# Optimization experiments

Measured on AMD Instinct MI355X. Metric: run time of the kernel, lower is better.

## Reference

```python
import jax, jax.numpy as jnp
import numpy as np

E = 100000    # number of edges
T = 1000000   # number of triplets
D = 128       # embed_dim
NB = 20       # n_basis (angle expansion width)
EPS = 1e-6


def setup_inputs() -> dict:
    key = jax.random.key(0)
    ks = jax.random.split(key, 14)
    def lin(k, fan_in, fan_out):
        # torch.nn.Linear default init: U(-1/sqrt(fan_in), 1/sqrt(fan_in))
        bound = 1.0 / np.sqrt(fan_in)
        kw, kb = jax.random.split(k)
        W = jax.random.uniform(kw, (fan_in, fan_out), jnp.float32, -bound, bound)
        b = jax.random.uniform(kb, (fan_out,), jnp.float32, -bound, bound)
        return W, b
    edge_attr = jax.random.normal(ks[0], (E, D), jnp.float32)
    edge_vectors = jax.random.normal(ks[1], (E, 3), jnp.float32)
    three_body_indices = jax.random.randint(ks[2], (T, 3), 0, 50000, jnp.int64)
    three_body_edge_indices = jax.random.randint(ks[3], (T, 2), 0, E, jnp.int64)
    Wa1, ba1 = lin(ks[4], 3, NB)          # SimpleMLPAngleExpansion layer 1
    Wa2, ba2 = lin(ks[5], NB, NB)         # SimpleMLPAngleExpansion layer 2
    W1, b1 = lin(ks[6], 2 * D + NB, D)    # phi_3b layer 1
    W2, b2 = lin(ks[7], D, D)             # phi_3b layer 2
    Wu, bu = lin(ks[8], D, D)             # update_edge
    return {
        "edge_attr": edge_attr,
        "three_body_indices": three_body_indices,
        "three_body_edge_indices": three_body_edge_indices,
        "edge_vectors": edge_vectors,
        "Wa1": Wa1, "ba1": ba1, "Wa2": Wa2, "ba2": ba2,
        "W1": W1, "b1": b1, "W2": W2, "b2": b2,
        "Wu": Wu, "bu": bu,
    }


def reference(edge_attr, three_body_indices, three_body_edge_indices, edge_vectors,
              Wa1, ba1, Wa2, ba2, W1, b1, W2, b2, Wu, bu):
    e_ij = three_body_edge_indices[:, 0]
    e_ik = three_body_edge_indices[:, 1]
    # gather edge vectors for the two edges forming the angle (sign-flipped)
    vec_ij = -edge_vectors[e_ij]           # (T, 3)
    vec_ik = -edge_vectors[e_ik]           # (T, 3)
    len_ij = jnp.maximum(jnp.linalg.norm(vec_ij, axis=1, keepdims=True), EPS)
    len_ik = jnp.maximum(jnp.linalg.norm(vec_ik, axis=1, keepdims=True), EPS)
    cos_t = jnp.clip(jnp.sum(vec_ij * vec_ik, axis=1, keepdims=True) / (len_ij * len_ik), -1.0, 1.0)
    # SimpleMLPAngleExpansion: (T,3) -> (T, NB)
    ang_in = jnp.concatenate([len_ij, len_ik, cos_t], axis=-1)
    angle_feats = jax.nn.silu(ang_in @ Wa1 + ba1) @ Wa2 + ba2
    # triplet features: gathered edge embeddings + angle features
    h_3b = jnp.concatenate([edge_attr[e_ij], edge_attr[e_ik], angle_feats], axis=-1)  # (T, 2D+NB)
    h_3b = jnp.nan_to_num(h_3b, nan=0.0, posinf=0.0, neginf=0.0)
    # phi_3b: Linear -> SiLU -> Linear
    m_ijk = jax.nn.silu(h_3b @ W1 + b1) @ W2 + b2   # (T, D)
    # scatter-add messages back to edge ij
    delta = jax.ops.segment_sum(m_ijk, e_ij, num_segments=edge_attr.shape[0])  # (E, D)
    return jnp.nan_to_num(delta @ Wu + bu, nan=0.0, posinf=0.0, neginf=0.0)
```

## Files before the change

kernel.cpp:

```cpp
#include <hip/hip_runtime.h>
#include <stdint.h>

#define NB 20

typedef __attribute__((ext_vector_type(8))) short bf16x8;
typedef __attribute__((ext_vector_type(4))) float f32x4;

__device__ __forceinline__ float bf_lo(uint32_t u) { return __uint_as_float(u << 16); }
__device__ __forceinline__ float bf_hi(uint32_t u) { return __uint_as_float(u & 0xffff0000u); }
__device__ __forceinline__ uint32_t f2bf(float f) {
    uint32_t u = __float_as_uint(f);
    return (u + 0x7fffu + ((u >> 16) & 1u)) >> 16;
}
__device__ __forceinline__ uint32_t pack_bf2(float a, float b) {
    return f2bf(a) | (f2bf(b) << 16);
}
__device__ __forceinline__ float silu_f(float x) {
    float e = __builtin_amdgcn_exp2f(-1.4426950408889634f * x);
    return x * __builtin_amdgcn_rcpf(1.f + e);
}

__global__ void prep_kernel(const float* __restrict__ W2, const float* __restrict__ b2,
                            const float* __restrict__ Wu,
                            float* __restrict__ Mf32, float* __restrict__ cvec) {
    int q = threadIdx.x;
    int k = blockIdx.x;
    const float* row = (k < 128) ? (W2 + k * 128) : b2;
    float acc0 = 0.f, acc1 = 0.f;
    for (int j = 0; j < 128; ++j) {
        float w = row[j];
        float2 wu = *(const float2*)(Wu + j * 128 + 2 * q);
        acc0 = fmaf(w, wu.x, acc0);
        acc1 = fmaf(w, wu.y, acc1);
    }
    if (k < 128) {
        Mf32[k * 128 + 2 * q] = acc0;
        Mf32[k * 128 + 2 * q + 1] = acc1;
    } else {
        cvec[2 * q] = acc0;
        cvec[2 * q + 1] = acc1;
    }
}

__global__ void prep2(const float* __restrict__ W1, uint32_t* __restrict__ Bpk) {
    int d = blockIdx.x * 256 + threadIdx.x;
    int q = d & 3, l = (d >> 2) & 63, c = (d >> 8) & 15, s = d >> 12;
    int k = 32 * s + ((l >> 4) << 3) + (q << 1);
    int col = (c << 4) + (l & 15);
    int r0 = (col < 128) ? k : (k + 128);
    int cc = col & 127;
    float v0 = W1[(size_t)r0 * 128 + cc];
    float v1 = W1[(size_t)(r0 + 1) * 128 + cc];
    Bpk[d] = pack_bf2(v0, v1);
}

__global__ void prepM(const float* __restrict__ Mf32, uint32_t* __restrict__ Mfrag) {
    int d = blockIdx.x * 256 + threadIdx.x;
    int q = d & 3, l = (d >> 2) & 63, c = (d >> 8) & 7, s = d >> 11;
    int k = 32 * s + ((l >> 4) << 3) + (q << 1);
    int col = (c << 4) + (l & 15);
    Mfrag[d] = pack_bf2(Mf32[k * 128 + col], Mf32[(k + 1) * 128 + col]);
}

__global__ void __launch_bounds__(256) kA3(const float* __restrict__ edge_attr,
                                           const uint32_t* __restrict__ Bpk,
                                           uint16_t* __restrict__ Pb, int E) {
    __shared__ uint32_t As[4096];
    __shared__ uint32_t Bs[16384];
    const int tid = threadIdx.x;
    const int e0 = blockIdx.x * 64;
    const int nE = min(64, E - e0);

    for (int d = tid; d < 4096; d += 256) {
        int row = d >> 6, p = d & 63;
        int g = p >> 2;
        float2 v;
        if (row < nE) v = *(const float2*)(edge_attr + (size_t)(e0 + row) * 128 + 2 * p);
        else { v.x = 0.f; v.y = 0.f; }
        As[row * 64 + ((g ^ (row & 7)) << 2) + (p & 3)] = pack_bf2(v.x, v.y);
    }
    for (int d = tid; d < 4096; d += 256)
        ((uint4*)Bs)[d] = ((const uint4*)Bpk)[d];
    __syncthreads();

    const int w = tid >> 6, l = tid & 63;

    bf16x8 afr[4][4];
#pragma unroll
    for (int rb = 0; rb < 4; ++rb)
#pragma unroll
        for (int s = 0; s < 4; ++s) {
            int row = rb * 16 + (l & 15);
            int g = s * 4 + (l >> 4);
            afr[rb][s] = *(const bf16x8*)((const char*)As + row * 256 + ((g ^ (row & 7)) << 4));
        }

    f32x4 acc[4][4];
#pragma unroll
    for (int cl = 0; cl < 4; ++cl)
#pragma unroll
        for (int rb = 0; rb < 4; ++rb) acc[cl][rb] = (f32x4)(0.f);

#pragma unroll
    for (int cl = 0; cl < 4; ++cl) {
        const int c = w * 4 + cl;
#pragma unroll
        for (int s = 0; s < 4; ++s) {
            bf16x8 bfr = *(const bf16x8*)((const char*)Bs + (((s * 16 + c) * 64 + l) << 4));
#pragma unroll
            for (int rb = 0; rb < 4; ++rb)
                acc[cl][rb] = __builtin_amdgcn_mfma_f32_16x16x32_bf16(afr[rb][s], bfr, acc[cl][rb], 0, 0, 0);
        }
    }

#pragma unroll
    for (int cl = 0; cl < 4; ++cl)
#pragma unroll
        for (int rb = 0; rb < 4; ++rb)
#pragma unroll
            for (int r = 0; r < 4; ++r) {
                int row = rb * 16 + (l >> 4) * 4 + r;
                if (row < nE)
                    Pb[(size_t)(e0 + row) * 256 + w * 64 + cl * 16 + (l & 15)] = (uint16_t)f2bf(acc[cl][rb][r]);
            }
}

__global__ void khist(const int* __restrict__ tbe, uint32_t* __restrict__ cnt, int T) {
    int t = blockIdx.x * blockDim.x + threadIdx.x;
    int stride = gridDim.x * blockDim.x;
    for (; t < T; t += stride) {
        int2 ee = ((const int2*)tbe)[t];
        atomicAdd(&cnt[ee.x], 1u);
    }
}

__global__ void scanA(const uint32_t* __restrict__ cnt, uint32_t* __restrict__ bsum, int E) {
    __shared__ uint32_t s[256];
    int tid = threadIdx.x;
    int e = blockIdx.x * 256 + tid;
    s[tid] = (e < E) ? cnt[e] : 0u;
    __syncthreads();
    for (int off = 128; off > 0; off >>= 1) {
        if (tid < off) s[tid] += s[tid + off];
        __syncthreads();
    }
    if (tid == 0) bsum[blockIdx.x] = s[0];
}

__global__ void scanB(uint32_t* __restrict__ bsum, int n) {
    __shared__ uint32_t s[512];
    int tid = threadIdx.x;
    s[tid] = (tid < n) ? bsum[tid] : 0u;
    __syncthreads();
    for (int off = 1; off < 512; off <<= 1) {
        uint32_t a = (tid >= off) ? s[tid - off] : 0u;
        __syncthreads();
        s[tid] += a;
        __syncthreads();
    }
    if (tid < n) bsum[tid] = (tid > 0) ? s[tid - 1] : 0u;
}

__global__ void scanC(const uint32_t* __restrict__ cnt, const uint32_t* __restrict__ bsum,
                      uint32_t* __restrict__ offs, int E) {
    __shared__ uint32_t s[256];
    int tid = threadIdx.x;
    int e = blockIdx.x * 256 + tid;
    uint32_t v = (e < E) ? cnt[e] : 0u;
    s[tid] = v;
    __syncthreads();
    for (int off = 1; off < 256; off <<= 1) {
        uint32_t a = (tid >= off) ? s[tid - off] : 0u;
        __syncthreads();
        s[tid] += a;
        __syncthreads();
    }
    if (e < E) offs[e] = bsum[blockIdx.x] + s[tid] - v;
}

__global__ void __launch_bounds__(256) kSA(const int* __restrict__ tbe,
                                           const float* __restrict__ evec,
                                           const float* __restrict__ Wa1,
                                           const float* __restrict__ ba1,
                                           const float* __restrict__ Wa2,
                                           const float* __restrict__ ba2,
                                           uint32_t* __restrict__ offs,
                                           uint32_t* __restrict__ afpk,
                                           uint32_t* __restrict__ sortedE2, int T) {
    __shared__ float wa1_s[60], ba1_s[NB], wa2_s[400], ba2_s[NB];
    const int tid = threadIdx.x;
    for (int i = tid; i < 400; i += 256) wa2_s[i] = Wa2[i];
    if (tid < 60) wa1_s[tid] = Wa1[tid];
    if (tid < NB) { ba1_s[tid] = ba1[tid]; ba2_s[tid] = ba2[tid]; }
    __syncthreads();

    const int t = blockIdx.x * 256 + tid;
    if (t >= T) return;

    int2 ee = ((const int2*)tbe)[t];
    const float ax = evec[ee.x * 3], ay = evec[ee.x * 3 + 1], az = evec[ee.x * 3 + 2];
    const float bx = evec[ee.y * 3], by = evec[ee.y * 3 + 1], bz = evec[ee.y * 3 + 2];
    const float li = fmaxf(__builtin_amdgcn_sqrtf(ax * ax + ay * ay + az * az), 1e-6f);
    const float lk = fmaxf(__builtin_amdgcn_sqrtf(bx * bx + by * by + bz * bz), 1e-6f);
    float ct = (ax * bx + ay * by + az * bz) * __builtin_amdgcn_rcpf(li * lk);
    ct = fminf(fmaxf(ct, -1.f), 1.f);

    float h[NB];
#pragma unroll
    for (int o = 0; o < NB; ++o) {
        float z = fmaf(li, wa1_s[o], fmaf(lk, wa1_s[20 + o], fmaf(ct, wa1_s[40 + o], ba1_s[o])));
        h[o] = silu_f(z);
    }
    float af[NB];
#pragma unroll
    for (int o2 = 0; o2 < NB; ++o2) af[o2] = ba2_s[o2];
#pragma unroll
    for (int o = 0; o < NB; ++o) {
#pragma unroll
        for (int o2 = 0; o2 < NB; ++o2) af[o2] = fmaf(h[o], wa2_s[o * 20 + o2], af[o2]);
    }

    const uint32_t pos = atomicAdd(&offs[ee.x], 1u);
    sortedE2[pos] = (uint32_t)ee.y;
    uint32_t* dst = afpk + (size_t)pos * 10;
#pragma unroll
    for (int j = 0; j < 5; ++j) {
        uint2 pk;
        pk.x = pack_bf2(af[4 * j], af[4 * j + 1]);
        pk.y = pack_bf2(af[4 * j + 2], af[4 * j + 3]);
        *(uint2*)(dst + 2 * j) = pk;
    }
}

__global__ void __launch_bounds__(256) kB5(const uint32_t* __restrict__ sortedE2,
                                           const uint32_t* __restrict__ offs,
                                           const float* __restrict__ W1,
                                           const float* __restrict__ b1,
                                           const uint32_t* __restrict__ Ppk,
                                           const uint32_t* __restrict__ afpk,
                                           float* __restrict__ S, int E) {
    __shared__ __align__(16) float af_s[4][64 * 20];
    __shared__ uint32_t e2_s[4][64];

    const int tid = threadIdx.x;
    const int wave = tid >> 6, lane = tid & 63;
    const int e = blockIdx.x * 4 + wave;
    if (e >= E) return;

    float2 wreg[NB];
#pragma unroll
    for (int k = 0; k < NB; ++k)
        wreg[k] = *(const float2*)(W1 + (size_t)(256 + k) * 128 + 2 * lane);

    const uint32_t start = (e > 0) ? offs[e - 1] : 0u;
    const uint32_t end = offs[e];
    const int n = (int)(end - start);

    const float2 b1v = ((const float2*)b1)[lane];
    const uint32_t p1 = Ppk[(size_t)e * 128 + lane];
    const float p1lo = bf_lo(p1) + b1v.x;
    const float p1hi = bf_hi(p1) + b1v.y;
    float acc0 = 0.f, acc1 = 0.f;

    float* afw = af_s[wave];

    for (int c0 = 0; c0 < n; c0 += 64) {
        const int m = min(64, n - c0);
        const uint32_t base10 = (start + c0) * 10u;
        for (int i = lane; i < m * 10; i += 64) {
            const uint32_t u = afpk[base10 + i];
            afw[2 * i] = bf_lo(u);
            afw[2 * i + 1] = bf_hi(u);
        }
        if (lane < m) e2_s[wave][lane] = sortedE2[start + c0 + lane];
        asm volatile("s_waitcnt lgkmcnt(0)" ::: "memory");
        __builtin_amdgcn_sched_barrier(0);

        uint32_t p2a = Ppk[(size_t)e2_s[wave][0] * 128 + 64 + lane];
        uint32_t p2b = (m > 1) ? Ppk[(size_t)e2_s[wave][1] * 128 + 64 + lane] : p2a;
        for (int i2 = 0; i2 < m; ++i2) {
            const uint32_t p2 = p2a;
            p2a = p2b;
            if (i2 + 2 < m) p2b = Ppk[(size_t)e2_s[wave][i2 + 2] * 128 + 64 + lane];
            float x0 = p1lo + bf_lo(p2);
            float x1 = p1hi + bf_hi(p2);
            const float4* afp = (const float4*)(afw + i2 * 20);
            const float4 fA = afp[0], fB = afp[1], fC = afp[2], fD = afp[3], fE = afp[4];
            const float a_[20] = {fA.x, fA.y, fA.z, fA.w, fB.x, fB.y, fB.z, fB.w,
                                  fC.x, fC.y, fC.z, fC.w, fD.x, fD.y, fD.z, fD.w,
                                  fE.x, fE.y, fE.z, fE.w};
#pragma unroll
            for (int j = 0; j < NB; ++j) {
                x0 = fmaf(a_[j], wreg[j].x, x0);
                x1 = fmaf(a_[j], wreg[j].y, x1);
            }
            acc0 += silu_f(x0);
            acc1 += silu_f(x1);
        }
    }
    float2 o;
    o.x = acc0;
    o.y = acc1;
    ((float2*)S)[(size_t)e * 64 + lane] = o;
}

__global__ void __launch_bounds__(256) kC2(const float* __restrict__ S,
                                           const uint32_t* __restrict__ Mfrag,
                                           const float* __restrict__ cvec,
                                           const float* __restrict__ bu,
                                           const uint32_t* __restrict__ cnt,
                                           int E) {
    __shared__ uint32_t As[4096];
    __shared__ uint32_t Bs[8192];
    __shared__ float cnt_s[64];
    const int tid = threadIdx.x;
    const int e0 = blockIdx.x * 64;
    const int nE = min(64, E - e0);

    for (int d = tid; d < 4096; d += 256) {
        int row = d >> 6, p = d & 63;
        int g = p >> 2;
        float2 v;
        if (row < nE) v = *(const float2*)(S + (size_t)(e0 + row) * 128 + 2 * p);
        else { v.x = 0.f; v.y = 0.f; }
        As[row * 64 + ((g ^ (row & 7)) << 2) + (p & 3)] = pack_bf2(v.x, v.y);
    }
    for (int d = tid; d < 2048; d += 256)
        ((uint4*)Bs)[d] = ((const uint4*)Mfrag)[d];
    if (tid < 64) cnt_s[tid] = (tid < nE) ? (float)cnt[e0 + tid] : 0.f;
    __syncthreads();

    const int w = tid >> 6, l = tid & 63;

    bf16x8 afr[4][4];
#pragma unroll
    for (int rb = 0; rb < 4; ++rb)
#pragma unroll
        for (int s = 0; s < 4; ++s) {
            int row = rb * 16 + (l & 15);
            int g = s * 4 + (l >> 4);
            afr[rb][s] = *(const bf16x8*)((const char*)As + row * 256 + ((g ^ (row & 7)) << 4));
        }

    f32x4 acc[2][4];
#pragma unroll
    for (int cl = 0; cl < 2; ++cl)
#pragma unroll
        for (int rb = 0; rb < 4; ++rb) acc[cl][rb] = (f32x4)(0.f);

#pragma unroll
    for (int cl = 0; cl < 2; ++cl) {
        const int c = w * 2 + cl;
#pragma unroll
        for (int s = 0; s < 4; ++s) {
            bf16x8 bfr = *(const bf16x8*)((const char*)Bs + (((s * 8 + c) * 64 + l) << 4));
#pragma unroll
            for (int rb = 0; rb < 4; ++rb)
                acc[cl][rb] = __builtin_amdgcn_mfma_f32_16x16x32_bf16(afr[rb][s], bfr, acc[cl][rb], 0, 0, 0);
        }
    }

#pragma unroll
    for (int cl = 0; cl < 2; ++cl) {
        const int col = w * 32 + cl * 16 + (l & 15);
        const float cv = cvec[col];
        const float bv = bu[col];
#pragma unroll
        for (int rb = 0; rb < 4; ++rb)
#pragma unroll
            for (int r = 0; r < 4; ++r) {
                int row = rb * 16 + (l >> 4) * 4 + r;
                if (row < nE) {
                    float* dst = (float*)S + (size_t)(e0 + row) * 128 + col;
                    *dst = acc[cl][rb][r] + fmaf(cnt_s[row], cv, bv);
                }
            }
    }
}

extern "C" void kernel_launch(void* const* d_in, const int* in_sizes, int n_in,
                              void* d_out, int out_size, void* d_ws, size_t ws_size,
                              hipStream_t stream) {
    const float* edge_attr = (const float*)d_in[0];
    const int* tbe = (const int*)d_in[2];
    const float* evec = (const float*)d_in[3];
    const float* Wa1 = (const float*)d_in[4];
    const float* ba1 = (const float*)d_in[5];
    const float* Wa2 = (const float*)d_in[6];
    const float* ba2 = (const float*)d_in[7];
    const float* W1 = (const float*)d_in[8];
    const float* b1 = (const float*)d_in[9];
    const float* W2 = (const float*)d_in[10];
    const float* b2 = (const float*)d_in[11];
    const float* Wu = (const float*)d_in[12];
    const float* bu = (const float*)d_in[13];

    const int E = in_sizes[0] / 128;
    const int T = in_sizes[2] / 2;
    float* S = (float*)d_out;

    const int nScanBlk = (E + 255) / 256;

    char* ws = (char*)d_ws;
    size_t off = 0;
    uint32_t* Ppk = (uint32_t*)(ws + off); off += (size_t)E * 512;
    uint32_t* cnt = (uint32_t*)(ws + off); off += (size_t)E * 4;
    uint32_t* offs = (uint32_t*)(ws + off); off += (size_t)E * 4;
    uint32_t* sortedE2 = (uint32_t*)(ws + off); off += (size_t)T * 4;
    uint32_t* afpk = (uint32_t*)(ws + off); off += (size_t)T * 40;
    uint32_t* bsum = (uint32_t*)(ws + off); off += (size_t)((nScanBlk + 3) & ~3) * 4;
    uint32_t* Bpk = (uint32_t*)(ws + off); off += 65536;
    float* Mf32 = (float*)(ws + off); off += 65536;
    uint32_t* Mfrag = (uint32_t*)(ws + off); off += 32768;
    float* cvec = (float*)(ws + off); off += 512;

    hipMemsetAsync(cnt, 0, (size_t)E * 4, stream);

    prep_kernel<<<129, 64, 0, stream>>>(W2, b2, Wu, Mf32, cvec);
    prep2<<<64, 256, 0, stream>>>(W1, Bpk);
    prepM<<<32, 256, 0, stream>>>(Mf32, Mfrag);
    kA3<<<(E + 63) / 64, 256, 0, stream>>>(edge_attr, Bpk, (uint16_t*)Ppk, E);
    khist<<<2048, 256, 0, stream>>>(tbe, cnt, T);
    scanA<<<nScanBlk, 256, 0, stream>>>(cnt, bsum, E);
    scanB<<<1, 512, 0, stream>>>(bsum, nScanBlk);
    scanC<<<nScanBlk, 256, 0, stream>>>(cnt, bsum, offs, E);
    kSA<<<(T + 255) / 256, 256, 0, stream>>>(tbe, evec, Wa1, ba1, Wa2, ba2,
                                             offs, afpk, sortedE2, T);
    kB5<<<(E + 3) / 4, 256, 0, stream>>>(sortedE2, offs, W1, b1, Ppk, afpk, S, E);
    kC2<<<(E + 63) / 64, 256, 0, stream>>>(S, Mfrag, cvec, bu, cnt, E);
}
```

Baseline: 518.5 us.

## Process 16 edges per wave in triplet kernel and gather angle features by triplet id

The per-triplet kernel now writes angle features at the triplet's original index and records a sorted list of triplet ids instead of the partner edge ids. The main accumulation kernel gives each wave a contiguous run of 16 edges and streams their triplets in chunks of 64 across edge boundaries, flushing each edge's accumulator when its segment ends. This is meant to stop waves idling on edges with few triplets and to make the atomic-scattered writes in the angle kernel coalesced. The cost is an indirect gather of angle features and partner ids through the triplet ids inside the hot kernel.

```diff
diff --git a/kernel.cpp b/kernel.cpp
--- a/kernel.cpp
+++ b/kernel.cpp
@@ -2,6 +2,7 @@
 #include <stdint.h>
 
 #define NB 20
+#define EG 16
 
 typedef __attribute__((ext_vector_type(8))) short bf16x8;
 typedef __attribute__((ext_vector_type(4))) float f32x4;
@@ -186,7 +187,7 @@
                                            const float* __restrict__ ba2,
                                            uint32_t* __restrict__ offs,
                                            uint32_t* __restrict__ afpk,
-                                           uint32_t* __restrict__ sortedE2, int T) {
+                                           uint32_t* __restrict__ sortedT, int T) {
     __shared__ float wa1_s[60], ba1_s[NB], wa2_s[400], ba2_s[NB];
     const int tid = threadIdx.x;
     for (int i = tid; i < 400; i += 256) wa2_s[i] = Wa2[i];
@@ -221,8 +222,8 @@
     }
 
     const uint32_t pos = atomicAdd(&offs[ee.x], 1u);
-    sortedE2[pos] = (uint32_t)ee.y;
-    uint32_t* dst = afpk + (size_t)pos * 10;
+    sortedT[pos] = (uint32_t)t;
+    uint32_t* dst = afpk + (size_t)t * 10;
 #pragma unroll
     for (int j = 0; j < 5; ++j) {
         uint2 pk;
@@ -232,8 +233,9 @@
     }
 }
 
-__global__ void __launch_bounds__(256) kB5(const uint32_t* __restrict__ sortedE2,
+__global__ void __launch_bounds__(256) kB6(const uint32_t* __restrict__ sortedT,
                                            const uint32_t* __restrict__ offs,
+                                           const int* __restrict__ tbe,
                                            const float* __restrict__ W1,
                                            const float* __restrict__ b1,
                                            const uint32_t* __restrict__ Ppk,
@@ -244,64 +246,106 @@
 
     const int tid = threadIdx.x;
     const int wave = tid >> 6, lane = tid & 63;
-    const int e = blockIdx.x * 4 + wave;
-    if (e >= E) return;
+    const int gw = blockIdx.x * 4 + wave;
+    const int eb = gw * EG;
+    if (eb >= E) return;
+    const int ee = min(eb + EG, E);
+
+    uint32_t offv = 0u;
+    {
+        int oi = eb - 1 + lane;
+        if (lane <= EG && oi >= 0) offv = offs[min(oi, E - 1)];
+    }
+    const uint32_t tstart = __shfl(offv, 0);
+    const uint32_t tend = __shfl(offv, ee - eb);
 
     float2 wreg[NB];
 #pragma unroll
     for (int k = 0; k < NB; ++k)
         wreg[k] = *(const float2*)(W1 + (size_t)(256 + k) * 128 + 2 * lane);
-
-    const uint32_t start = (e > 0) ? offs[e - 1] : 0u;
-    const uint32_t end = offs[e];
-    const int n = (int)(end - start);
-
     const float2 b1v = ((const float2*)b1)[lane];
-    const uint32_t p1 = Ppk[(size_t)e * 128 + lane];
-    const float p1lo = bf_lo(p1) + b1v.x;
-    const float p1hi = bf_hi(p1) + b1v.y;
+
+    int ecur = eb;
+    uint32_t eend = __shfl(offv, 1);
+    uint32_t p1A = Ppk[(size_t)ecur * 128 + lane];
+    uint32_t p1B = Ppk[(size_t)min(ecur + 1, E - 1) * 128 + lane];
+    float p1lo = bf_lo(p1A) + b1v.x;
+    float p1hi = bf_hi(p1A) + b1v.y;
     float acc0 = 0.f, acc1 = 0.f;
 
     float* afw = af_s[wave];
 
-    for (int c0 = 0; c0 < n; c0 += 64) {
-        const int m = min(64, n - c0);
-        const uint32_t base10 = (start + c0) * 10u;
-        for (int i = lane; i < m * 10; i += 64) {
-            const uint32_t u = afpk[base10 + i];
+    for (uint32_t base = tstart; base < tend; base += 64u) {
+        const int m = min(64, (int)(tend - base));
+        const uint32_t idx = min(base + (uint32_t)lane, tend - 1u);
+        const uint32_t st = sortedT[idx];
+        e2_s[wave][lane] = (uint32_t)(((const int2*)tbe)[st].y);
+#pragma unroll
+        for (int k = 0; k < 10; ++k) {
+            int i = lane + 64 * k;
+            int r = i / 10;
+            int c = i - r * 10;
+            uint32_t str = __shfl(st, r);
+            uint32_t u = afpk[(size_t)str * 10 + c];
             afw[2 * i] = bf_lo(u);
             afw[2 * i + 1] = bf_hi(u);
         }
-        if (lane < m) e2_s[wave][lane] = sortedE2[start + c0 + lane];
         asm volatile("s_waitcnt lgkmcnt(0)" ::: "memory");
         __builtin_amdgcn_sched_barrier(0);
 
         uint32_t p2a = Ppk[(size_t)e2_s[wave][0] * 128 + 64 + lane];
         uint32_t p2b = (m > 1) ? Ppk[(size_t)e2_s[wave][1] * 128 + 64 + lane] : p2a;
-        for (int i2 = 0; i2 < m; ++i2) {
-            const uint32_t p2 = p2a;
-            p2a = p2b;
-            if (i2 + 2 < m) p2b = Ppk[(size_t)e2_s[wave][i2 + 2] * 128 + 64 + lane];
-            float x0 = p1lo + bf_lo(p2);
-            float x1 = p1hi + bf_hi(p2);
-            const float4* afp = (const float4*)(afw + i2 * 20);
-            const float4 fA = afp[0], fB = afp[1], fC = afp[2], fD = afp[3], fE = afp[4];
-            const float a_[20] = {fA.x, fA.y, fA.z, fA.w, fB.x, fB.y, fB.z, fB.w,
-                                  fC.x, fC.y, fC.z, fC.w, fD.x, fD.y, fD.z, fD.w,
-                                  fE.x, fE.y, fE.z, fE.w};
-#pragma unroll
-            for (int j = 0; j < NB; ++j) {
-                x0 = fmaf(a_[j], wreg[j].x, x0);
-                x1 = fmaf(a_[j], wreg[j].y, x1);
+        int i2 = 0;
+        while (i2 < m) {
+            const uint32_t rem = eend - base;
+            const int lim = (rem < (uint32_t)m) ? (int)rem : m;
+            for (; i2 < lim; ++i2) {
+                const uint32_t p2 = p2a;
+                p2a = p2b;
+                if (i2 + 2 < m) p2b = Ppk[(size_t)e2_s[wave][i2 + 2] * 128 + 64 + lane];
+                float x0 = p1lo + bf_lo(p2);
+                float x1 = p1hi + bf_hi(p2);
+                const float4* afp = (const float4*)(afw + i2 * 20);
+                const float4 fA = afp[0], fB = afp[1], fC = afp[2], fD = afp[3], fE = afp[4];
+                const float a_[20] = {fA.x, fA.y, fA.z, fA.w, fB.x, fB.y, fB.z, fB.w,
+                                      fC.x, fC.y, fC.z, fC.w, fD.x, fD.y, fD.z, fD.w,
+                                      fE.x, fE.y, fE.z, fE.w};
+#pragma unroll
+                for (int j = 0; j < NB; ++j) {
+                    x0 = fmaf(a_[j], wreg[j].x, x0);
+                    x1 = fmaf(a_[j], wreg[j].y, x1);
+                }
+                acc0 += silu_f(x0);
+                acc1 += silu_f(x1);
             }
-            acc0 += silu_f(x0);
-            acc1 += silu_f(x1);
-        }
-    }
-    float2 o;
-    o.x = acc0;
-    o.y = acc1;
-    ((float2*)S)[(size_t)e * 64 + lane] = o;
+            if (base + (uint32_t)i2 == eend) {
+                do {
+                    float2 o;
+                    o.x = acc0;
+                    o.y = acc1;
+                    ((float2*)S)[(size_t)ecur * 64 + lane] = o;
+                    acc0 = 0.f;
+                    acc1 = 0.f;
+                    ++ecur;
+                    if (ecur >= ee) { eend = 0xffffffffu; break; }
+                    p1A = p1B;
+                    p1B = Ppk[(size_t)min(ecur + 1, E - 1) * 128 + lane];
+                    p1lo = bf_lo(p1A) + b1v.x;
+                    p1hi = bf_hi(p1A) + b1v.y;
+                    eend = __shfl(offv, ecur - eb + 1);
+                } while (base + (uint32_t)i2 == eend);
+            }
+        }
+    }
+    while (ecur < ee) {
+        float2 o;
+        o.x = acc0;
+        o.y = acc1;
+        ((float2*)S)[(size_t)ecur * 64 + lane] = o;
+        acc0 = 0.f;
+        acc1 = 0.f;
+        ++ecur;
+    }
 }
 
 __global__ void __launch_bounds__(256) kC2(const float* __restrict__ S,
@@ -406,7 +450,7 @@
     uint32_t* Ppk = (uint32_t*)(ws + off); off += (size_t)E * 512;
     uint32_t* cnt = (uint32_t*)(ws + off); off += (size_t)E * 4;
     uint32_t* offs = (uint32_t*)(ws + off); off += (size_t)E * 4;
-    uint32_t* sortedE2 = (uint32_t*)(ws + off); off += (size_t)T * 4;
+    uint32_t* sortedT = (uint32_t*)(ws + off); off += (size_t)T * 4;
     uint32_t* afpk = (uint32_t*)(ws + off); off += (size_t)T * 40;
     uint32_t* bsum = (uint32_t*)(ws + off); off += (size_t)((nScanBlk + 3) & ~3) * 4;
     uint32_t* Bpk = (uint32_t*)(ws + off); off += 65536;
@@ -425,7 +469,8 @@
     scanB<<<1, 512, 0, stream>>>(bsum, nScanBlk);
     scanC<<<nScanBlk, 256, 0, stream>>>(cnt, bsum, offs, E);
     kSA<<<(T + 255) / 256, 256, 0, stream>>>(tbe, evec, Wa1, ba1, Wa2, ba2,
-                                             offs, afpk, sortedE2, T);
-    kB5<<<(E + 3) / 4, 256, 0, stream>>>(sortedE2, offs, W1, b1, Ppk, afpk, S, E);
+                                             offs, afpk, sortedT, T);
+    const int nWaves = (E + EG - 1) / EG;
+    kB6<<<(nWaves + 3) / 4, 256, 0, stream>>>(sortedT, offs, tbe, W1, b1, Ppk, afpk, S, E);
     kC2<<<(E + 63) / 64, 256, 0, stream>>>(S, Mfrag, cvec, bu, cnt, E);
 }
```

Measured after the change: 562.9 us. 8.6% more time.
